# Kernel tuning notes

Measured on AMD Instinct MI355X. Metric: run time of the kernel, lower is better.

## Reference

```python
import jax, jax.numpy as jnp
import numpy as np

B, N, D, H, NW = 16, 400, 256, 8, 4
DH = D // H
EPS_LN = 1e-5

def _layer_norm(x, g, b):
    m = jnp.mean(x, axis=-1, keepdims=True)
    v = jnp.mean((x - m) ** 2, axis=-1, keepdims=True)
    return (x - m) / jnp.sqrt(v + EPS_LN) * g + b

def setup_inputs() -> dict:
    key = jax.random.key(0)
    ks = jax.random.split(key, 10)
    p = lambda k, shape: (jax.random.normal(k, shape, jnp.float32) * 0.02)
    return {
        'x': jax.random.normal(ks[0], (B, N, D), jnp.float32),
        'attention_weights': jax.random.normal(ks[1], (B, NW, N, N), jnp.float32),
        'Wq': p(ks[2], (D, D)), 'bq': jnp.zeros((D,), jnp.float32),
        'Wk': p(ks[3], (D, D)), 'bk': jnp.zeros((D,), jnp.float32),
        'Wv': p(ks[4], (D, D)), 'bv': jnp.zeros((D,), jnp.float32),
        'Wo': p(ks[5], (D, D)), 'bo': jnp.zeros((D,), jnp.float32),
        'g1': jnp.ones((D,), jnp.float32), 'beta1': jnp.zeros((D,), jnp.float32),
        'W1': p(ks[6], (4 * D, D)), 'b1': jnp.zeros((4 * D,), jnp.float32),
        'W2': p(ks[7], (D, 4 * D)), 'b2': jnp.zeros((D,), jnp.float32),
        'g2': jnp.ones((D,), jnp.float32), 'beta2': jnp.zeros((D,), jnp.float32),
    }

def reference(x, attention_weights, Wq, bq, Wk, bk, Wv, bv, Wo, bo,
              g1, beta1, W1, b1, W2, b2, g2, beta2):
    b, n, d = x.shape
    # QKV projections, split heads: [B, H, N, DH]
    q = (x @ Wq.T + bq).reshape(b, n, H, DH).transpose(0, 2, 1, 3)
    k = (x @ Wk.T + bk).reshape(b, n, H, DH).transpose(0, 2, 1, 3)
    v = (x @ Wv.T + bv).reshape(b, n, H, DH).transpose(0, 2, 1, 3)
    qk = jnp.einsum('bhnd,bhmd->bhnm', q, k) / np.sqrt(DH)  # [B,H,N,N]
    # signed attention averaged over the NW per-sample weight matrices
    nw = attention_weights.shape[1]
    scores = jnp.zeros_like(qk)
    for i in range(nw):  # small fixed count, not a data dim
        w = attention_weights[:, i][:, None, :, :]  # [B,1,N,N]
        s = qk * w
        e = jnp.exp(jnp.abs(s))
        scores = scores + jnp.sign(s) * e / (jnp.sum(e, axis=-1, keepdims=True) + 1e-10)
    scores = scores / nw
    attn_out = jnp.einsum('bhnm,bhmd->bhnd', scores, v)
    attn_out = attn_out.transpose(0, 2, 1, 3).reshape(b, n, d)
    attn_out = attn_out @ Wo.T + bo
    h = _layer_norm(x + attn_out, g1, beta1)
    ffn = jax.nn.relu(h @ W1.T + b1) @ W2.T + b2
    y = _layer_norm(h + ffn, g2, beta2)
    return (y, scores)
```

## Files before the change

### kernel.cpp

```cpp
#include <hip/hip_runtime.h>
#include <hip/hip_fp16.h>

typedef unsigned int uint32;

#define B_ 16
#define N_ 400
#define D_ 256
#define H_ 8
#define DH_ 32
#define NW_ 4

#if __has_builtin(__builtin_amdgcn_exp2f)
#define EXP2(x) __builtin_amdgcn_exp2f(x)
#else
#define EXP2(x) exp2f(x)
#endif

#define QK_SCL 0.2550348f

using bf16x8 = __attribute__((ext_vector_type(8))) short;
using f16x8  = __attribute__((ext_vector_type(8))) _Float16;
using f32x4  = __attribute__((ext_vector_type(4))) float;

__device__ __forceinline__ ushort f2b(float f) {
  uint32 u = __float_as_uint(f);
  uint32 r = (u + 0x7fffu + ((u >> 16) & 1u)) >> 16;
  return (ushort)r;
}

__global__ __launch_bounds__(256) void convert_kernel(
    const float* __restrict__ x,  const float* __restrict__ wq,
    const float* __restrict__ wk, const float* __restrict__ wv,
    const float* __restrict__ wo, const float* __restrict__ w1,
    const float* __restrict__ w2,
    ushort* __restrict__ xb,  ushort* __restrict__ wqb,
    ushort* __restrict__ wkb, ushort* __restrict__ wvb,
    ushort* __restrict__ wob, ushort* __restrict__ w1b,
    ushort* __restrict__ w2b) {
  int gid = blockIdx.x * 256 + threadIdx.x;
  const float* src; ushort* dst;
  if      (gid < 409600) { src = x;  dst = xb;  }
  else if ((gid -= 409600) < 16384) { src = wq; dst = wqb; }
  else if ((gid -= 16384) < 16384)  { src = wk; dst = wkb; }
  else if ((gid -= 16384) < 16384)  { src = wv; dst = wvb; }
  else if ((gid -= 16384) < 16384)  { src = wo; dst = wob; }
  else if ((gid -= 16384) < 65536)  { src = w1; dst = w1b; }
  else { gid -= 65536; src = w2; dst = w2b; }
  float4 f = ((const float4*)src)[gid];
  ushort4 u;
  u.x = f2b(f.x); u.y = f2b(f.y); u.z = f2b(f.z); u.w = f2b(f.w);
  *(ushort4*)&dst[(size_t)gid * 4] = u;
}

template <int RELU, int RESID, int OUT_F32, int OUT_BF16>
__global__ __launch_bounds__(256) void gemm_bt(
    const ushort* __restrict__ A, const ushort* __restrict__ W,
    const float* __restrict__ bias, const float* __restrict__ resid,
    float* __restrict__ outf, ushort* __restrict__ outb,
    int M, int N, int K) {
  __shared__ __align__(16) ushort As[2][64 * 40];
  __shared__ __align__(16) ushort Ws[2][64 * 40];
  int t = threadIdx.x;
  int l = t & 63, w = t >> 6;
  int n0 = blockIdx.x * 64, m0 = blockIdx.y * 64;
  int srow = t >> 2, sc = (t & 3) * 8;
  int lrow = l & 15, lk = (l >> 4) * 8;

  const uint4* ag = (const uint4*)&A[(size_t)(m0 + srow) * K + sc];
  const uint4* wg = (const uint4*)&W[(size_t)(n0 + srow) * K + sc];
  uint4 ar = ag[0], wr = wg[0];
  int nk = K >> 5;

  f32x4 acc[4];
#pragma unroll
  for (int nt = 0; nt < 4; nt++) acc[nt] = {0.f, 0.f, 0.f, 0.f};

  for (int kk = 0; kk < nk; kk++) {
    int cur = kk & 1;
    *(uint4*)&As[cur][srow * 40 + sc] = ar;
    *(uint4*)&Ws[cur][srow * 40 + sc] = wr;
    if (kk + 1 < nk) { ar = ag[(size_t)(kk + 1) * 4]; wr = wg[(size_t)(kk + 1) * 4]; }
    __syncthreads();
    bf16x8 af = *(const bf16x8*)&As[cur][(16 * w + lrow) * 40 + lk];
#pragma unroll
    for (int nt = 0; nt < 4; nt++) {
      bf16x8 bf = *(const bf16x8*)&Ws[cur][(nt * 16 + lrow) * 40 + lk];
      acc[nt] = __builtin_amdgcn_mfma_f32_16x16x32_bf16(af, bf, acc[nt], 0, 0, 0);
    }
  }

#pragma unroll
  for (int nt = 0; nt < 4; nt++) {
    int n = n0 + nt * 16 + lrow;
    float bv = bias[n];
#pragma unroll
    for (int r = 0; r < 4; r++) {
      int m = m0 + 16 * w + (l >> 4) * 4 + r;
      float v = acc[nt][r] + bv;
      if (RELU)  v = fmaxf(v, 0.f);
      if (RESID) v += resid[(size_t)m * N + n];
      if (OUT_F32)  outf[(size_t)m * N + n] = v;
      if (OUT_BF16) outb[(size_t)m * N + n] = f2b(v);
    }
  }
}

__global__ __launch_bounds__(256) void qkv_gemm(
    const ushort* __restrict__ xb, const ushort* __restrict__ wq,
    const ushort* __restrict__ wk, const ushort* __restrict__ wv,
    const float* __restrict__ bq, const float* __restrict__ bk,
    const float* __restrict__ bv,
    _Float16* __restrict__ qh, _Float16* __restrict__ kh,
    _Float16* __restrict__ vt) {
  __shared__ __align__(16) ushort As[2][64 * 40];
  __shared__ __align__(16) ushort Ws[2][64 * 40];
  int z = blockIdx.z;
  const ushort* W = (z == 0) ? wq : (z == 1) ? wk : wv;
  const float* bias = (z == 0) ? bq : (z == 1) ? bk : bv;

  int t = threadIdx.x;
  int l = t & 63, w = t >> 6;
  int n0 = blockIdx.x * 64, m0 = blockIdx.y * 64;
  int srow = t >> 2, sc = (t & 3) * 8;
  int lrow = l & 15, lk = (l >> 4) * 8;

  const uint4* ag = (const uint4*)&xb[(size_t)(m0 + srow) * 256 + sc];
  const uint4* wg = (const uint4*)&W[(size_t)(n0 + srow) * 256 + sc];
  uint4 ar = ag[0], wr = wg[0];

  f32x4 acc[4];
#pragma unroll
  for (int nt = 0; nt < 4; nt++) acc[nt] = {0.f, 0.f, 0.f, 0.f};

  for (int kk = 0; kk < 8; kk++) {
    int cur = kk & 1;
    *(uint4*)&As[cur][srow * 40 + sc] = ar;
    *(uint4*)&Ws[cur][srow * 40 + sc] = wr;
    if (kk + 1 < 8) { ar = ag[(kk + 1) * 4]; wr = wg[(kk + 1) * 4]; }
    __syncthreads();
    bf16x8 af = *(const bf16x8*)&As[cur][(16 * w + lrow) * 40 + lk];
#pragma unroll
    for (int nt = 0; nt < 4; nt++) {
      bf16x8 bf = *(const bf16x8*)&Ws[cur][(nt * 16 + lrow) * 40 + lk];
      acc[nt] = __builtin_amdgcn_mfma_f32_16x16x32_bf16(af, bf, acc[nt], 0, 0, 0);
    }
  }

  int mb = m0 + 16 * w + (l >> 4) * 4;
  int bb = mb / 400;
  int mi = mb - bb * 400;
#pragma unroll
  for (int nt = 0; nt < 4; nt++) {
    int n = n0 + nt * 16 + lrow;
    float bvv = bias[n];
    if (z < 2) {
      _Float16* out = z ? kh : qh;
      float scl = z ? 1.f : QK_SCL;
      int hh = n >> 5, dd = n & 31;
      _Float16* dst = out + (((size_t)(bb * 8 + hh)) * 400 + mi) * 32 + dd;
#pragma unroll
      for (int r = 0; r < 4; r++)
        dst[(size_t)r * 32] = (_Float16)((acc[nt][r] + bvv) * scl);
    } else {
      _Float16 h4[4];
#pragma unroll
      for (int r = 0; r < 4; r++) h4[r] = (_Float16)(acc[nt][r] + bvv);
      *(uint2*)&vt[((size_t)bb * 256 + n) * 400 + mi] = *(uint2*)h4;
    }
  }
}

#define SP 416

__global__ __launch_bounds__(256) void attn_kernel(
    const _Float16* __restrict__ qh, const _Float16* __restrict__ kh,
    const _Float16* __restrict__ vt, const float* __restrict__ aw,
    float* __restrict__ scores, ushort* __restrict__ attnb) {
  __shared__ __align__(16) char smem[16 * SP * 2 + 256];
  __half* S = (__half*)smem;
  float* zin = (float*)(smem + 16 * SP * 2);

  int id = blockIdx.x;
  int c = ((id >> 6) << 3) | (id & 7);
  int hh = (id >> 3) & 7;
  int b = c / 25;
  int n0 = (c - b * 25) * 16;

  int t = threadIdx.x;
  int w = t >> 6, l = t & 63;
  int lq = l >> 4, lr = l & 15;

  {
    const _Float16* qbase = qh + (((size_t)(b * 8 + hh)) * 400 + n0) * 32;
    const _Float16* kbase = kh + ((size_t)(b * 8 + hh)) * 400 * 32;
    f16x8 af = *(const f16x8*)(qbase + lr * 32 + lq * 8);
    for (int mt = w; mt < 25; mt += 4) {
      f16x8 bf = *(const f16x8*)(kbase + (size_t)(mt * 16 + lr) * 32 + lq * 8);
      f32x4 cc = {0.f, 0.f, 0.f, 0.f};
      cc = __builtin_amdgcn_mfma_f32_16x16x32_f16(af, bf, cc, 0, 0, 0);
#pragma unroll
      for (int r = 0; r < 4; r++)
        S[(lq * 4 + r) * SP + mt * 16 + lr] = __float2half(cc[r]);
    }
  }
  __syncthreads();

  {
    int r = t >> 2, p = t & 3;
    int i = r >> 4, n = r & 15;
    const float* wrow = aw + (((size_t)(b * 4 + i)) * 400 + n0 + n) * 400;
    const __half* srow = S + n * SP;
    float z = 0.f;
    for (int m = p * 4; m < 400; m += 16) {
      float4 wv = *(const float4*)(wrow + m);
      float2 f0 = __half22float2(*(const __half2*)(srow + m));
      float2 f1 = __half22float2(*(const __half2*)(srow + m + 2));
      z += EXP2(fabsf(f0.x * wv.x)) + EXP2(fabsf(f0.y * wv.y)) +
           EXP2(fabsf(f1.x * wv.z)) + EXP2(fabsf(f1.y * wv.w));
    }
    z += __shfl_xor(z, 1);
    z += __shfl_xor(z, 2);
    if (p == 0) zin[r] = 0.25f / (z + 1e-10f);
  }
  __syncthreads();

  {
    int n = t >> 4, p = t & 15;
    float zz[4] = {zin[n], zin[16 + n], zin[32 + n], zin[48 + n]};
    __half* srow = S + n * SP;
    const float* awn = aw + (((size_t)(b * 4)) * 400 + n0 + n) * 400;
    float* scout = scores + (((size_t)(b * 8 + hh)) * 400 + n0 + n) * 400;
    for (int m = p * 4; m < 448; m += 64) {
      if (m < 400) {
        float2 f0 = __half22float2(*(const __half2*)(srow + m));
        float2 f1 = __half22float2(*(const __half2*)(srow + m + 2));
        float q0 = f0.x, q1 = f0.y, q2 = f1.x, q3 = f1.y;
        float s0 = 0.f, s1 = 0.f, s2 = 0.f, s3 = 0.f;
#pragma unroll
        for (int i = 0; i < 4; i++) {
          float4 wv = *(const float4*)(awn + (size_t)i * 160000 + m);
          float t0 = q0 * wv.x; s0 += copysignf(EXP2(fabsf(t0)) * zz[i], t0);
          float t1 = q1 * wv.y; s1 += copysignf(EXP2(fabsf(t1)) * zz[i], t1);
          float t2 = q2 * wv.z; s2 += copysignf(EXP2(fabsf(t2)) * zz[i], t2);
          float t3 = q3 * wv.w; s3 += copysignf(EXP2(fabsf(t3)) * zz[i], t3);
        }
        float4 o = {s0, s1, s2, s3};
        *(float4*)(scout + m) = o;
        __half h4[4] = {__float2half(s0), __float2half(s1),
                        __float2half(s2), __float2half(s3)};
        *(uint2*)(srow + m) = *(uint2*)h4;
      } else if (m < 416) {
        uint2 zero = {0u, 0u};
        *(uint2*)(srow + m) = zero;
      }
    }
  }
  __syncthreads();

  const _Float16* vbase = vt + (((size_t)b) * 256 + hh * 32) * 400;
  f32x4 a0 = {0.f, 0.f, 0.f, 0.f}, a1 = {0.f, 0.f, 0.f, 0.f};
  const _Float16* Sh = (const _Float16*)S;
  for (int c2 = w; c2 < 13; c2 += 4) {
    f16x8 sf = *(const f16x8*)(Sh + lr * SP + c2 * 32 + lq * 8);
    f16x8 v0 = *(const f16x8*)(vbase + (size_t)lr * 400 + c2 * 32 + lq * 8);
    f16x8 v1 = *(const f16x8*)(vbase + (size_t)(16 + lr) * 400 + c2 * 32 + lq * 8);
    a0 = __builtin_amdgcn_mfma_f32_16x16x32_f16(sf, v0, a0, 0, 0, 0);
    a1 = __builtin_amdgcn_mfma_f32_16x16x32_f16(sf, v1, a1, 0, 0, 0);
  }
  __syncthreads();
  float* Of = (float*)smem;
#pragma unroll
  for (int r = 0; r < 4; r++) {
    Of[(w * 16 + lq * 4 + r) * 32 + lr] = a0[r];
    Of[(w * 16 + lq * 4 + r) * 32 + 16 + lr] = a1[r];
  }
  __syncthreads();
  for (int o = t; o < 512; o += 256) {
    int n = o >> 5, d = o & 31;
    float s = Of[n * 32 + d] + Of[512 + n * 32 + d] +
              Of[1024 + n * 32 + d] + Of[1536 + n * 32 + d];
    attnb[((size_t)(b * 400 + n0 + n)) * 256 + hh * 32 + d] = f2b(s);
  }
}

__global__ __launch_bounds__(256) void ln_kernel(
    const float* __restrict__ src, const float* __restrict__ g,
    const float* __restrict__ be, float* __restrict__ outf,
    ushort* __restrict__ outb) {
  int row = blockIdx.x, t = threadIdx.x;
  float v = src[(size_t)row * 256 + t];
  __shared__ float red[4];
  float s = v;
#pragma unroll
  for (int o = 32; o > 0; o >>= 1) s += __shfl_down(s, o, 64);
  if ((t & 63) == 0) red[t >> 6] = s;
  __syncthreads();
  float mean = (red[0] + red[1] + red[2] + red[3]) * (1.f / 256.f);
  __syncthreads();
  float d = v - mean;
  s = d * d;
#pragma unroll
  for (int o = 32; o > 0; o >>= 1) s += __shfl_down(s, o, 64);
  if ((t & 63) == 0) red[t >> 6] = s;
  __syncthreads();
  float var = (red[0] + red[1] + red[2] + red[3]) * (1.f / 256.f);
  float y = d * rsqrtf(var + 1e-5f) * g[t] + be[t];
  outf[(size_t)row * 256 + t] = y;
  if (outb) outb[(size_t)row * 256 + t] = f2b(y);
}

extern "C" void kernel_launch(void* const* d_in, const int* in_sizes, int n_in,
                              void* d_out, int out_size, void* d_ws,
                              size_t ws_size, hipStream_t stream) {
  const float* x   = (const float*)d_in[0];
  const float* aw  = (const float*)d_in[1];
  const float* Wq  = (const float*)d_in[2];
  const float* bq  = (const float*)d_in[3];
  const float* Wk  = (const float*)d_in[4];
  const float* bk  = (const float*)d_in[5];
  const float* Wv  = (const float*)d_in[6];
  const float* bv  = (const float*)d_in[7];
  const float* Wo  = (const float*)d_in[8];
  const float* bo  = (const float*)d_in[9];
  const float* g1  = (const float*)d_in[10];
  const float* be1 = (const float*)d_in[11];
  const float* W1  = (const float*)d_in[12];
  const float* b1  = (const float*)d_in[13];
  const float* W2  = (const float*)d_in[14];
  const float* b2  = (const float*)d_in[15];
  const float* g2  = (const float*)d_in[16];
  const float* be2 = (const float*)d_in[17];

  if (ws_size < 34340864) return;

  char* ws = (char*)d_ws;
  ushort*   xb    = (ushort*)(ws + 0);
  ushort*   wqb   = (ushort*)(ws + 3276800);
  ushort*   wkb   = (ushort*)(ws + 3407872);
  ushort*   wvb   = (ushort*)(ws + 3538944);
  ushort*   wob   = (ushort*)(ws + 3670016);
  ushort*   w1b   = (ushort*)(ws + 3801088);
  ushort*   w2b   = (ushort*)(ws + 4325376);
  _Float16* qhb   = (_Float16*)(ws + 4849664);
  _Float16* khb   = (_Float16*)(ws + 8126464);
  _Float16* vtb   = (_Float16*)(ws + 11403264);
  ushort*   attnb = (ushort*)(ws + 14680064);
  float*    ao    = (float*)(ws + 17956864);
  float*    hbuf  = (float*)(ws + 24510464);
  ushort*   hb    = (ushort*)(ws + 31064064);
  ushort*   ffn1b = (ushort*)qhb;
  float*    ffn2  = ao;

  float* yout   = (float*)d_out;
  float* scores = yout + 1638400;

  convert_kernel<<<2368, 256, 0, stream>>>(x, Wq, Wk, Wv, Wo, W1, W2,
                                           xb, wqb, wkb, wvb, wob, w1b, w2b);
  qkv_gemm<<<dim3(4, 100, 3), 256, 0, stream>>>(
      xb, wqb, wkb, wvb, bq, bk, bv, qhb, khb, vtb);
  attn_kernel<<<3200, 256, 0, stream>>>(qhb, khb, vtb, aw, scores, attnb);
  gemm_bt<0, 1, 1, 0><<<dim3(4, 100), 256, 0, stream>>>(
      attnb, wob, bo, x, ao, nullptr, 6400, 256, 256);
  ln_kernel<<<6400, 256, 0, stream>>>(ao, g1, be1, hbuf, hb);
  gemm_bt<1, 0, 0, 1><<<dim3(16, 100), 256, 0, stream>>>(
      hb, w1b, b1, nullptr, nullptr, ffn1b, 6400, 1024, 256);
  gemm_bt<0, 1, 1, 0><<<dim3(4, 100), 256, 0, stream>>>(
      ffn1b, w2b, b2, hbuf, ffn2, nullptr, 6400, 256, 1024);
  ln_kernel<<<6400, 256, 0, stream>>>(ffn2, g2, be2, yout, nullptr);
}
```

Baseline: 272.1 us.

## Fuse out-projection, both LayerNorms and FFN into one row-tile tail kernel

Result: slower. 294.0 us (+8.1%).

```diff
diff --git a/kernel.cpp b/kernel.cpp
--- a/kernel.cpp
+++ b/kernel.cpp
@@ -26,6 +26,9 @@
   uint32 u = __float_as_uint(f);
   uint32 r = (u + 0x7fffu + ((u >> 16) & 1u)) >> 16;
   return (ushort)r;
+}
+__device__ __forceinline__ float b2f(ushort u) {
+  return __uint_as_float(((uint32)u) << 16);
 }
 
 __global__ __launch_bounds__(256) void convert_kernel(
@@ -52,59 +55,6 @@
   *(ushort4*)&dst[(size_t)gid * 4] = u;
 }
 
-template <int RELU, int RESID, int OUT_F32, int OUT_BF16>
-__global__ __launch_bounds__(256) void gemm_bt(
-    const ushort* __restrict__ A, const ushort* __restrict__ W,
-    const float* __restrict__ bias, const float* __restrict__ resid,
-    float* __restrict__ outf, ushort* __restrict__ outb,
-    int M, int N, int K) {
-  __shared__ __align__(16) ushort As[2][64 * 40];
-  __shared__ __align__(16) ushort Ws[2][64 * 40];
-  int t = threadIdx.x;
-  int l = t & 63, w = t >> 6;
-  int n0 = blockIdx.x * 64, m0 = blockIdx.y * 64;
-  int srow = t >> 2, sc = (t & 3) * 8;
-  int lrow = l & 15, lk = (l >> 4) * 8;
-
-  const uint4* ag = (const uint4*)&A[(size_t)(m0 + srow) * K + sc];
-  const uint4* wg = (const uint4*)&W[(size_t)(n0 + srow) * K + sc];
-  uint4 ar = ag[0], wr = wg[0];
-  int nk = K >> 5;
-
-  f32x4 acc[4];
-#pragma unroll
-  for (int nt = 0; nt < 4; nt++) acc[nt] = {0.f, 0.f, 0.f, 0.f};
-
-  for (int kk = 0; kk < nk; kk++) {
-    int cur = kk & 1;
-    *(uint4*)&As[cur][srow * 40 + sc] = ar;
-    *(uint4*)&Ws[cur][srow * 40 + sc] = wr;
-    if (kk + 1 < nk) { ar = ag[(size_t)(kk + 1) * 4]; wr = wg[(size_t)(kk + 1) * 4]; }
-    __syncthreads();
-    bf16x8 af = *(const bf16x8*)&As[cur][(16 * w + lrow) * 40 + lk];
-#pragma unroll
-    for (int nt = 0; nt < 4; nt++) {
-      bf16x8 bf = *(const bf16x8*)&Ws[cur][(nt * 16 + lrow) * 40 + lk];
-      acc[nt] = __builtin_amdgcn_mfma_f32_16x16x32_bf16(af, bf, acc[nt], 0, 0, 0);
-    }
-  }
-
-#pragma unroll
-  for (int nt = 0; nt < 4; nt++) {
-    int n = n0 + nt * 16 + lrow;
-    float bv = bias[n];
-#pragma unroll
-    for (int r = 0; r < 4; r++) {
-      int m = m0 + 16 * w + (l >> 4) * 4 + r;
-      float v = acc[nt][r] + bv;
-      if (RELU)  v = fmaxf(v, 0.f);
-      if (RESID) v += resid[(size_t)m * N + n];
-      if (OUT_F32)  outf[(size_t)m * N + n] = v;
-      if (OUT_BF16) outb[(size_t)m * N + n] = f2b(v);
-    }
-  }
-}
-
 __global__ __launch_bounds__(256) void qkv_gemm(
     const ushort* __restrict__ xb, const ushort* __restrict__ wq,
     const ushort* __restrict__ wk, const ushort* __restrict__ wv,
@@ -283,30 +233,187 @@
   }
 }
 
-__global__ __launch_bounds__(256) void ln_kernel(
-    const float* __restrict__ src, const float* __restrict__ g,
-    const float* __restrict__ be, float* __restrict__ outf,
-    ushort* __restrict__ outb) {
-  int row = blockIdx.x, t = threadIdx.x;
-  float v = src[(size_t)row * 256 + t];
-  __shared__ float red[4];
-  float s = v;
-#pragma unroll
-  for (int o = 32; o > 0; o >>= 1) s += __shfl_down(s, o, 64);
-  if ((t & 63) == 0) red[t >> 6] = s;
-  __syncthreads();
-  float mean = (red[0] + red[1] + red[2] + red[3]) * (1.f / 256.f);
-  __syncthreads();
-  float d = v - mean;
-  s = d * d;
-#pragma unroll
-  for (int o = 32; o > 0; o >>= 1) s += __shfl_down(s, o, 64);
-  if ((t & 63) == 0) red[t >> 6] = s;
-  __syncthreads();
-  float var = (red[0] + red[1] + red[2] + red[3]) * (1.f / 256.f);
-  float y = d * rsqrtf(var + 1e-5f) * g[t] + be[t];
-  outf[(size_t)row * 256 + t] = y;
-  if (outb) outb[(size_t)row * 256 + t] = f2b(y);
+#define HP 272
+#define RP 1040
+
+__global__ __launch_bounds__(512, 2) void tail_kernel(
+    const ushort* __restrict__ attnb, const ushort* __restrict__ wob,
+    const float* __restrict__ bo, const float* __restrict__ x,
+    const float* __restrict__ g1, const float* __restrict__ be1,
+    const ushort* __restrict__ w1b, const float* __restrict__ b1,
+    const ushort* __restrict__ w2b, const float* __restrict__ b2,
+    const float* __restrict__ g2, const float* __restrict__ be2,
+    float* __restrict__ yout) {
+  __shared__ __align__(16) ushort bufA[16 * HP];
+  __shared__ __align__(16) ushort relu[16 * RP];
+  __shared__ float lnS[16 * 8], lnQ[16 * 8];
+
+  int m0 = blockIdx.x * 16;
+  int t = threadIdx.x, w = t >> 6, l = t & 63;
+  int lr = l & 15, lq = l >> 4;
+  int row4 = lq * 4;
+
+  {
+    int row = t >> 5, c = (t & 31) * 8;
+    *(uint4*)&bufA[row * HP + c] =
+        *(const uint4*)&attnb[(size_t)(m0 + row) * 256 + c];
+  }
+  __syncthreads();
+
+  f32x4 acc[2];
+  acc[0] = {0.f, 0.f, 0.f, 0.f}; acc[1] = {0.f, 0.f, 0.f, 0.f};
+  for (int ks = 0; ks < 8; ks++) {
+    bf16x8 af = *(const bf16x8*)&bufA[lr * HP + ks * 32 + lq * 8];
+#pragma unroll
+    for (int nt = 0; nt < 2; nt++) {
+      bf16x8 bf = *(const bf16x8*)&wob[(size_t)(w * 32 + nt * 16 + lr) * 256 +
+                                       ks * 32 + lq * 8];
+      acc[nt] = __builtin_amdgcn_mfma_f32_16x16x32_bf16(af, bf, acc[nt], 0, 0, 0);
+    }
+  }
+  float vals[2][4];
+  float rs[4] = {0.f, 0.f, 0.f, 0.f}, rq[4] = {0.f, 0.f, 0.f, 0.f};
+#pragma unroll
+  for (int nt = 0; nt < 2; nt++) {
+    int n = w * 32 + nt * 16 + lr;
+    float bon = bo[n];
+#pragma unroll
+    for (int r = 0; r < 4; r++) {
+      float v = acc[nt][r] + bon + x[(size_t)(m0 + row4 + r) * 256 + n];
+      vals[nt][r] = v;
+      rs[r] += v; rq[r] += v * v;
+    }
+  }
+#pragma unroll
+  for (int r = 0; r < 4; r++) {
+#pragma unroll
+    for (int o = 1; o < 16; o <<= 1) {
+      rs[r] += __shfl_xor(rs[r], o);
+      rq[r] += __shfl_xor(rq[r], o);
+    }
+  }
+  if (lr == 0) {
+#pragma unroll
+    for (int r = 0; r < 4; r++) {
+      lnS[(row4 + r) * 8 + w] = rs[r];
+      lnQ[(row4 + r) * 8 + w] = rq[r];
+    }
+  }
+  __syncthreads();
+  {
+    float mean[4], rsig[4];
+#pragma unroll
+    for (int r = 0; r < 4; r++) {
+      int m = row4 + r;
+      float s = 0.f, q = 0.f;
+#pragma unroll
+      for (int j = 0; j < 8; j++) { s += lnS[m * 8 + j]; q += lnQ[m * 8 + j]; }
+      float mu = s * (1.f / 256.f);
+      float va = q * (1.f / 256.f) - mu * mu;
+      mean[r] = mu; rsig[r] = rsqrtf(va + 1e-5f);
+    }
+#pragma unroll
+    for (int nt = 0; nt < 2; nt++) {
+      int n = w * 32 + nt * 16 + lr;
+      float g = g1[n], be = be1[n];
+#pragma unroll
+      for (int r = 0; r < 4; r++) {
+        float h = (vals[nt][r] - mean[r]) * rsig[r] * g + be;
+        bufA[(row4 + r) * HP + n] = f2b(h);
+      }
+    }
+  }
+  __syncthreads();
+
+  {
+    f32x4 a1[8];
+#pragma unroll
+    for (int nt = 0; nt < 8; nt++) a1[nt] = {0.f, 0.f, 0.f, 0.f};
+    for (int ks = 0; ks < 8; ks++) {
+      bf16x8 af = *(const bf16x8*)&bufA[lr * HP + ks * 32 + lq * 8];
+#pragma unroll
+      for (int nt = 0; nt < 8; nt++) {
+        bf16x8 bf = *(const bf16x8*)&w1b[(size_t)(w * 128 + nt * 16 + lr) * 256 +
+                                         ks * 32 + lq * 8];
+        a1[nt] = __builtin_amdgcn_mfma_f32_16x16x32_bf16(af, bf, a1[nt], 0, 0, 0);
+      }
+    }
+#pragma unroll
+    for (int nt = 0; nt < 8; nt++) {
+      int n = w * 128 + nt * 16 + lr;
+      float bn = b1[n];
+#pragma unroll
+      for (int r = 0; r < 4; r++) {
+        float v = fmaxf(a1[nt][r] + bn, 0.f);
+        relu[(row4 + r) * RP + n] = f2b(v);
+      }
+    }
+  }
+  __syncthreads();
+
+  f32x4 a2[2];
+  a2[0] = {0.f, 0.f, 0.f, 0.f}; a2[1] = {0.f, 0.f, 0.f, 0.f};
+  for (int ks = 0; ks < 32; ks++) {
+    bf16x8 af = *(const bf16x8*)&relu[lr * RP + ks * 32 + lq * 8];
+#pragma unroll
+    for (int nt = 0; nt < 2; nt++) {
+      bf16x8 bf = *(const bf16x8*)&w2b[(size_t)(w * 32 + nt * 16 + lr) * 1024 +
+                                       ks * 32 + lq * 8];
+      a2[nt] = __builtin_amdgcn_mfma_f32_16x16x32_bf16(af, bf, a2[nt], 0, 0, 0);
+    }
+  }
+  float vals2[2][4];
+  float rs2[4] = {0.f, 0.f, 0.f, 0.f}, rq2[4] = {0.f, 0.f, 0.f, 0.f};
+#pragma unroll
+  for (int nt = 0; nt < 2; nt++) {
+    int n = w * 32 + nt * 16 + lr;
+    float bn = b2[n];
+#pragma unroll
+    for (int r = 0; r < 4; r++) {
+      float v = a2[nt][r] + bn + b2f(bufA[(row4 + r) * HP + n]);
+      vals2[nt][r] = v;
+      rs2[r] += v; rq2[r] += v * v;
+    }
+  }
+#pragma unroll
+  for (int r = 0; r < 4; r++) {
+#pragma unroll
+    for (int o = 1; o < 16; o <<= 1) {
+      rs2[r] += __shfl_xor(rs2[r], o);
+      rq2[r] += __shfl_xor(rq2[r], o);
+    }
+  }
+  if (lr == 0) {
+#pragma unroll
+    for (int r = 0; r < 4; r++) {
+      lnS[(row4 + r) * 8 + w] = rs2[r];
+      lnQ[(row4 + r) * 8 + w] = rq2[r];
+    }
+  }
+  __syncthreads();
+  {
+    float mean[4], rsig[4];
+#pragma unroll
+    for (int r = 0; r < 4; r++) {
+      int m = row4 + r;
+      float s = 0.f, q = 0.f;
+#pragma unroll
+      for (int j = 0; j < 8; j++) { s += lnS[m * 8 + j]; q += lnQ[m * 8 + j]; }
+      float mu = s * (1.f / 256.f);
+      float va = q * (1.f / 256.f) - mu * mu;
+      mean[r] = mu; rsig[r] = rsqrtf(va + 1e-5f);
+    }
+#pragma unroll
+    for (int nt = 0; nt < 2; nt++) {
+      int n = w * 32 + nt * 16 + lr;
+      float g = g2[n], be = be2[n];
+#pragma unroll
+      for (int r = 0; r < 4; r++) {
+        float y = (vals2[nt][r] - mean[r]) * rsig[r] * g + be;
+        yout[(size_t)(m0 + row4 + r) * 256 + n] = y;
+      }
+    }
+  }
 }
 
 extern "C" void kernel_launch(void* const* d_in, const int* in_sizes, int n_in,
@@ -345,11 +452,6 @@
   _Float16* khb   = (_Float16*)(ws + 8126464);
   _Float16* vtb   = (_Float16*)(ws + 11403264);
   ushort*   attnb = (ushort*)(ws + 14680064);
-  float*    ao    = (float*)(ws + 17956864);
-  float*    hbuf  = (float*)(ws + 24510464);
-  ushort*   hb    = (ushort*)(ws + 31064064);
-  ushort*   ffn1b = (ushort*)qhb;
-  float*    ffn2  = ao;
 
   float* yout   = (float*)d_out;
   float* scores = yout + 1638400;
@@ -359,12 +461,6 @@
   qkv_gemm<<<dim3(4, 100, 3), 256, 0, stream>>>(
       xb, wqb, wkb, wvb, bq, bk, bv, qhb, khb, vtb);
   attn_kernel<<<3200, 256, 0, stream>>>(qhb, khb, vtb, aw, scores, attnb);
-  gemm_bt<0, 1, 1, 0><<<dim3(4, 100), 256, 0, stream>>>(
-      attnb, wob, bo, x, ao, nullptr, 6400, 256, 256);
-  ln_kernel<<<6400, 256, 0, stream>>>(ao, g1, be1, hbuf, hb);
-  gemm_bt<1, 0, 0, 1><<<dim3(16, 100), 256, 0, stream>>>(
-      hb, w1b, b1, nullptr, nullptr, ffn1b, 6400, 1024, 256);
-  gemm_bt<0, 1, 1, 0><<<dim3(4, 100), 256, 0, stream>>>(
-      ffn1b, w2b, b2, hbuf, ffn2, nullptr, 6400, 256, 1024);
-  ln_kernel<<<6400, 256, 0, stream>>>(ffn2, g2, be2, yout, nullptr);
-}
+  tail_kernel<<<400, 512, 0, stream>>>(attnb, wob, bo, x, g1, be1,
+                                       w1b, b1, w2b, b2, g2, be2, yout);
+}
```
